# Performance work log

Hardware: AMD Instinct MI355X
Metric: run time of the kernel (lower is better)

## Reference

```python
import jax, jax.numpy as jnp
import numpy as np

N_NODES = 50000
N_EDGES = 800000
C = 96
L = 3


def setup_inputs() -> dict:
    key = jax.random.key(0)
    ks = jax.random.split(key, 7)
    x = jax.random.normal(ks[0], (N_NODES, C), dtype=jnp.float32)
    edge_index = jax.random.randint(ks[1], (2, N_EDGES), 0, N_NODES, dtype=jnp.int32)
    weight = jax.random.normal(ks[2], (L, C, C), dtype=jnp.float32) * (1.0 / np.sqrt(C))
    w_ih = jax.random.normal(ks[3], (3 * C, C), dtype=jnp.float32) * (1.0 / np.sqrt(C))
    w_hh = jax.random.normal(ks[4], (3 * C, C), dtype=jnp.float32) * (1.0 / np.sqrt(C))
    b_ih = jax.random.normal(ks[5], (3 * C,), dtype=jnp.float32) * 0.01
    b_hh = jax.random.normal(ks[6], (3 * C,), dtype=jnp.float32) * 0.01
    return {"x": x, "edge_index": edge_index, "weight": weight,
            "w_ih": w_ih, "w_hh": w_hh, "b_ih": b_ih, "b_hh": b_hh}


def _gru_cell(m, h, w_ih, w_hh, b_ih, b_hh):
    # PyTorch GRUCell math. gi/gh: [N, 3C]
    gi = m @ w_ih.T + b_ih
    gh = h @ w_hh.T + b_hh
    i_r, i_z, i_n = jnp.split(gi, 3, axis=-1)
    h_r, h_z, h_n = jnp.split(gh, 3, axis=-1)
    r = jax.nn.sigmoid(i_r + h_r)
    z = jax.nn.sigmoid(i_z + h_z)
    n = jnp.tanh(i_n + r * h_n)
    return (1.0 - z) * n + z * h


def reference(x, edge_index, weight, w_ih, w_hh, b_ih, b_hh):
    src = edge_index[0]  # message source (x_j)
    dst = edge_index[1]  # aggregation target
    for i in range(L):
        m = x @ weight[i]                                        # [N, C]
        agg = jax.ops.segment_sum(m[src], dst, num_segments=N_NODES)  # scatter-add
        x = _gru_cell(agg, x, w_ih, w_hh, b_ih, b_hh)
    return x
```

## Files before the change

### kernel.cpp

```cpp
#include <hip/hip_runtime.h>
#include <hip/hip_bf16.h>
#include <stdint.h>

#define NN 50000
#define NE 800000
#define CC 96
#define NL 3
#define NMT 3125

#define CAP 64
#define CAPSH 6

#define ELEMS_PER_LAYER 55296

#define FILL_GROUPS 8
#define FILL_GROUP_BLOCKS 400
#define FILL_BLOCKS (FILL_GROUPS*FILL_GROUP_BLOCKS)
#define NODES_PER_GROUP (NN/FILL_GROUPS)

#define PREP_ITEMS (NN*CC/8 + NL*288*CC + 288*CC)
#define PREP_BLOCKS ((PREP_ITEMS + 255)/256)

typedef _Float16 f16x8 __attribute__((ext_vector_type(8)));
typedef float f32x4 __attribute__((ext_vector_type(4)));
typedef uint16_t u16x8 __attribute__((ext_vector_type(8)));

__device__ __forceinline__ uint16_t f2h(float f){
  _Float16 h = (_Float16)f;
  return __builtin_bit_cast(uint16_t, h);
}
__device__ __forceinline__ float h2f(uint16_t u){
  return (float)__builtin_bit_cast(_Float16, u);
}

__device__ __forceinline__ size_t frag_elem(int tcol, int g2, int ks, int lane, int j){
  return (((size_t)(tcol*6 + g2)*3 + ks)*64 + lane)*8 + j;
}

__global__ void k_setup(const int* __restrict__ srcv, const int* __restrict__ dstv,
                        int* __restrict__ cursor, uint16_t* __restrict__ ssrc,
                        const float4* __restrict__ x, u16x8* __restrict__ xh,
                        const float* __restrict__ weight, const float* __restrict__ w_ih,
                        const float* __restrict__ w_hh, uint16_t* __restrict__ gw){
  if(blockIdx.x < FILL_BLOCKS){
    int g  = blockIdx.x & 7;
    int bg = blockIdx.x >> 3;
    int dlo = g * NODES_PER_GROUP;
    int dhi = dlo + NODES_PER_GROUP;
    const int tpg = FILL_GROUP_BLOCKS*256;
    for(int e = bg*256 + threadIdx.x; e < NE; e += tpg){
      int d = dstv[e];
      if(d >= dlo && d < dhi){
        int s = srcv[e];
        int pos = atomicAdd(&cursor[d], 1);
        if(pos < CAP) ssrc[((size_t)d << CAPSH) + pos] = (uint16_t)s;
      }
    }
    return;
  }
  int idx = (blockIdx.x - FILL_BLOCKS)*256 + threadIdx.x;
  const int N8 = NN*CC/8;
  if(idx < N8){
    float4 a = x[idx*2], b = x[idx*2+1];
    u16x8 o;
    o[0]=f2h(a.x); o[1]=f2h(a.y); o[2]=f2h(a.z); o[3]=f2h(a.w);
    o[4]=f2h(b.x); o[5]=f2h(b.y); o[6]=f2h(b.z); o[7]=f2h(b.w);
    xh[idx] = o;
    return;
  }
  int pidx = idx - N8;
  const int TOT1 = NL*288*CC;
  const int TOT2 = 288*CC;
  if(pidx < TOT1){
    int k = pidx % CC;
    int col = (pidx / CC) % 288;
    int l = pidx / (CC*288);
    const float4* wr = (const float4*)(weight + (size_t)(l*CC + k)*CC);
    const float4* ir = (const float4*)(w_ih + (size_t)col*CC);
    float acc = 0.f;
    #pragma unroll 4
    for(int k2=0;k2<CC/4;k2++){
      float4 a = wr[k2], b = ir[k2];
      acc += a.x*b.x + a.y*b.y + a.z*b.z + a.w*b.w;
    }
    int g = col / 96, cg = col % 96;
    int tcol = cg >> 4, n = cg & 15;
    int ks = k >> 5, r = (k & 31) >> 3, j = k & 7;
    int lane = r*16 + n;
    gw[(size_t)l*ELEMS_PER_LAYER + frag_elem(tcol, g, ks, lane, j)] = f2h(acc);
  } else {
    int idx2 = pidx - TOT1;
    if(idx2 < TOT2){
      int k = idx2 % CC;
      int col = idx2 / CC;
      uint16_t h = f2h(w_hh[(size_t)col*CC + k]);
      int g = col / 96, cg = col % 96;
      int tcol = cg >> 4, n = cg & 15;
      int ks = k >> 5, r = (k & 31) >> 3, j = k & 7;
      int lane = r*16 + n;
      size_t fe = frag_elem(tcol, 3+g, ks, lane, j);
      #pragma unroll
      for(int l=0;l<NL;l++) gw[(size_t)l*ELEMS_PER_LAYER + fe] = h;
    }
  }
}

__global__ void k_aggregate(const u16x8* __restrict__ xh,
                            const int* __restrict__ counts, const uint16_t* __restrict__ ssrc,
                            u16x8* __restrict__ s16){
  int tid = blockIdx.x*256 + threadIdx.x;
  if(tid >= NN*12) return;
  int n = tid / 12;
  int c8 = tid - n*12;
  int cnt = counts[n];
  if(cnt > CAP) cnt = CAP;
  int o0 = n << CAPSH;
  int o1 = o0 + cnt;
  float a[8];
  #pragma unroll
  for(int t=0;t<8;t++) a[t] = 0.f;
  int j = o0;
  for(; j+8 <= o1; j+=8){
    int s0 = ssrc[j],   s1 = ssrc[j+1], s2 = ssrc[j+2], s3 = ssrc[j+3];
    int s4 = ssrc[j+4], s5 = ssrc[j+5], s6 = ssrc[j+6], s7 = ssrc[j+7];
    u16x8 v0 = xh[(size_t)s0*12 + c8];
    u16x8 v1 = xh[(size_t)s1*12 + c8];
    u16x8 v2 = xh[(size_t)s2*12 + c8];
    u16x8 v3 = xh[(size_t)s3*12 + c8];
    u16x8 v4 = xh[(size_t)s4*12 + c8];
    u16x8 v5 = xh[(size_t)s5*12 + c8];
    u16x8 v6 = xh[(size_t)s6*12 + c8];
    u16x8 v7 = xh[(size_t)s7*12 + c8];
    #pragma unroll
    for(int t=0;t<8;t++)
      a[t] += ((h2f(v0[t])+h2f(v1[t]))+(h2f(v2[t])+h2f(v3[t])))
            + ((h2f(v4[t])+h2f(v5[t]))+(h2f(v6[t])+h2f(v7[t])));
  }
  for(; j < o1; j++){
    u16x8 v = xh[(size_t)ssrc[j]*12 + c8];
    #pragma unroll
    for(int t=0;t<8;t++) a[t] += h2f(v[t]);
  }
  u16x8 o;
  #pragma unroll
  for(int t=0;t<8;t++) o[t] = f2h(a[t]);
  s16[tid] = o;
}

#define MFMA16(A,B,C) __builtin_amdgcn_mfma_f32_16x16x32_f16(A,B,C,0,0,0)

__global__ __launch_bounds__(1024) void k_gru(
    const uint16_t* __restrict__ s16, uint16_t* xh,
    const uint16_t* __restrict__ gw_l,
    const float* __restrict__ b_ih, const float* __restrict__ b_hh,
    float* __restrict__ out_f)
{
  __shared__ __align__(16) uint16_t lw[ELEMS_PER_LAYER];

  const int tid = threadIdx.x;
  int wave = tid >> 6;
  int lane = tid & 63;
  int mtile = wave*256 + blockIdx.x;
  bool valid = (mtile < NMT);
  int mt = valid ? mtile : 0;
  int nidx = lane & 15;
  int quad = lane >> 4;

  f16x8 as[3], ax[3];
  {
    size_t arow = (size_t)(mt*16 + nidx)*CC;
    #pragma unroll
    for(int ks=0; ks<3; ks++){
      int ko = ks*32 + quad*8;
      as[ks] = *reinterpret_cast<const f16x8*>(s16 + arow + ko);
      ax[ks] = *reinterpret_cast<const f16x8*>(xh + arow + ko);
    }
  }

  {
    const uint4* src = (const uint4*)gw_l;
    uint4* dst = (uint4*)lw;
    #pragma unroll
    for(int i=0;i<7;i++){
      int chunk = i*1024 + tid;
      if(chunk < ELEMS_PER_LAYER/8) dst[chunk] = src[chunk];
    }
  }
  __syncthreads();
  if(!valid) return;

  #pragma unroll 1
  for(int tcol=0; tcol<6; tcol++){
    f32x4 air = {0.f,0.f,0.f,0.f}, aiz = {0.f,0.f,0.f,0.f}, ain = {0.f,0.f,0.f,0.f};
    f32x4 ahr = {0.f,0.f,0.f,0.f}, ahz = {0.f,0.f,0.f,0.f}, ahn = {0.f,0.f,0.f,0.f};

    #pragma unroll
    for(int ks=0; ks<3; ks++){
      const uint16_t* base = lw + (((size_t)tcol*6)*3 + ks)*512 + lane*8;
      #define BFRAG(g2) (*reinterpret_cast<const f16x8*>(base + (size_t)(g2)*3*512))
      air = MFMA16(as[ks], BFRAG(0), air);
      aiz = MFMA16(as[ks], BFRAG(1), aiz);
      ain = MFMA16(as[ks], BFRAG(2), ain);
      ahr = MFMA16(ax[ks], BFRAG(3), ahr);
      ahz = MFMA16(ax[ks], BFRAG(4), ahz);
      ahn = MFMA16(ax[ks], BFRAG(5), ahn);
      #undef BFRAG
    }

    int c = tcol*16 + nidx;
    float bir_ = b_ih[c], biz_ = b_ih[CC+c], bin_ = b_ih[2*CC+c];
    float bhr_ = b_hh[c], bhz_ = b_hh[CC+c], bhn_ = b_hh[2*CC+c];

    #pragma unroll
    for(int r=0;r<4;r++){
      int node = mtile*16 + quad*4 + r;
      float ir  = air[r] + bir_;
      float iz  = aiz[r] + biz_;
      float in_ = ain[r] + bin_;
      float hr  = ahr[r] + bhr_;
      float hz  = ahz[r] + bhz_;
      float hn  = ahn[r] + bhn_;
      float rg = 1.f/(1.f + __expf(-(ir+hr)));
      float zg = 1.f/(1.f + __expf(-(iz+hz)));
      float nv = in_ + rg*hn;
      float av = fminf(fabsf(nv), 15.f);
      float e2 = __expf(2.f*av);
      float tg = 1.f - 2.f/(e2 + 1.f);
      tg = (nv < 0.f)? -tg : tg;
      size_t oi = (size_t)node*CC + c;
      float hp = h2f(xh[oi]);
      float h = (1.f - zg)*tg + zg*hp;
      if(out_f) out_f[oi] = h;
      else      xh[oi] = f2h(h);
    }
  }
}

extern "C" void kernel_launch(void* const* d_in, const int* in_sizes, int n_in,
                              void* d_out, int out_size, void* d_ws, size_t ws_size,
                              hipStream_t stream){
  const float* x0     = (const float*)d_in[0];
  const int*   ei     = (const int*)d_in[1];
  const float* weight = (const float*)d_in[2];
  const float* w_ih   = (const float*)d_in[3];
  const float* w_hh   = (const float*)d_in[4];
  const float* b_ih   = (const float*)d_in[5];
  const float* b_hh   = (const float*)d_in[6];
  float* out = (float*)d_out;

  const int* srcv = ei;
  const int* dstv = ei + NE;

  char* ws = (char*)d_ws;
  size_t off = 0;
  auto carve = [&](size_t bytes)->char*{
    char* p = ws + off;
    off += (bytes + 255) & ~(size_t)255;
    return p;
  };
  int* cursor    = (int*)carve((size_t)NN*4);
  uint16_t* ssrc = (uint16_t*)carve((size_t)NN*CAP*2);
  uint16_t* s16  = (uint16_t*)carve((size_t)NN*CC*2);
  uint16_t* xh   = (uint16_t*)carve((size_t)NN*CC*2);
  uint16_t* gw   = (uint16_t*)carve((size_t)NL*ELEMS_PER_LAYER*2);

  hipMemsetAsync(cursor, 0, (size_t)NN*4, stream);
  k_setup<<<FILL_BLOCKS + PREP_BLOCKS, 256, 0, stream>>>(
      srcv, dstv, cursor, ssrc, (const float4*)x0, (u16x8*)xh, weight, w_ih, w_hh, gw);

  for(int l=0; l<NL; l++){
    k_aggregate<<<((NN*12)+255)/256, 256, 0, stream>>>(
        (const u16x8*)xh, cursor, ssrc, (u16x8*)s16);
    float* out_f = (l==NL-1) ? out : nullptr;
    k_gru<<<256, 1024, 0, stream>>>(s16, xh,
                                    gw + (size_t)l*ELEMS_PER_LAYER,
                                    b_ih, b_hh, out_f);
  }
}
```

Baseline: 275.7 us.

## Fuse neighbor aggregation into GRU layer kernel with ping-pong node buffers

Removes the separate aggregation kernel and performs the gather-sum inside the GRU kernel. Each thread sums three 8-channel chunks for one node, staging the results in shared memory as MFMA A-fragments. This avoids writing and re-reading the aggregated fp16 buffer in global memory and saves one launch per layer. Because other blocks still read the current node states while this layer writes new ones, the states now alternate between two buffers. The trade-off is fewer waves for the latency-bound gather and shared memory use close to the per-CU limit.

Result: faster. 256.6 us (-6.9%).

```diff
diff --git a/kernel.cpp b/kernel.cpp
--- a/kernel.cpp
+++ b/kernel.cpp
@@ -105,76 +105,33 @@
   }
 }
 
-__global__ void k_aggregate(const u16x8* __restrict__ xh,
-                            const int* __restrict__ counts, const uint16_t* __restrict__ ssrc,
-                            u16x8* __restrict__ s16){
-  int tid = blockIdx.x*256 + threadIdx.x;
-  if(tid >= NN*12) return;
-  int n = tid / 12;
-  int c8 = tid - n*12;
-  int cnt = counts[n];
-  if(cnt > CAP) cnt = CAP;
-  int o0 = n << CAPSH;
-  int o1 = o0 + cnt;
-  float a[8];
-  #pragma unroll
-  for(int t=0;t<8;t++) a[t] = 0.f;
-  int j = o0;
-  for(; j+8 <= o1; j+=8){
-    int s0 = ssrc[j],   s1 = ssrc[j+1], s2 = ssrc[j+2], s3 = ssrc[j+3];
-    int s4 = ssrc[j+4], s5 = ssrc[j+5], s6 = ssrc[j+6], s7 = ssrc[j+7];
-    u16x8 v0 = xh[(size_t)s0*12 + c8];
-    u16x8 v1 = xh[(size_t)s1*12 + c8];
-    u16x8 v2 = xh[(size_t)s2*12 + c8];
-    u16x8 v3 = xh[(size_t)s3*12 + c8];
-    u16x8 v4 = xh[(size_t)s4*12 + c8];
-    u16x8 v5 = xh[(size_t)s5*12 + c8];
-    u16x8 v6 = xh[(size_t)s6*12 + c8];
-    u16x8 v7 = xh[(size_t)s7*12 + c8];
-    #pragma unroll
-    for(int t=0;t<8;t++)
-      a[t] += ((h2f(v0[t])+h2f(v1[t]))+(h2f(v2[t])+h2f(v3[t])))
-            + ((h2f(v4[t])+h2f(v5[t]))+(h2f(v6[t])+h2f(v7[t])));
-  }
-  for(; j < o1; j++){
-    u16x8 v = xh[(size_t)ssrc[j]*12 + c8];
-    #pragma unroll
-    for(int t=0;t<8;t++) a[t] += h2f(v[t]);
-  }
-  u16x8 o;
-  #pragma unroll
-  for(int t=0;t<8;t++) o[t] = f2h(a[t]);
-  s16[tid] = o;
-}
-
 #define MFMA16(A,B,C) __builtin_amdgcn_mfma_f32_16x16x32_f16(A,B,C,0,0,0)
 
-__global__ __launch_bounds__(1024) void k_gru(
-    const uint16_t* __restrict__ s16, uint16_t* xh,
+__global__ __launch_bounds__(1024) void k_layer(
+    const uint16_t* __restrict__ xh_cur, uint16_t* __restrict__ xh_nxt,
+    const int* __restrict__ counts, const uint16_t* __restrict__ ssrc,
     const uint16_t* __restrict__ gw_l,
     const float* __restrict__ b_ih, const float* __restrict__ b_hh,
     float* __restrict__ out_f)
 {
   __shared__ __align__(16) uint16_t lw[ELEMS_PER_LAYER];
+  __shared__ u16x8 aggl[12*256];
 
   const int tid = threadIdx.x;
-  int wave = tid >> 6;
-  int lane = tid & 63;
-  int mtile = wave*256 + blockIdx.x;
-  bool valid = (mtile < NMT);
-  int mt = valid ? mtile : 0;
-  int nidx = lane & 15;
-  int quad = lane >> 4;
-
-  f16x8 as[3], ax[3];
+  const int wave = tid >> 6;
+  const int lane = tid & 63;
+  const int nidx = lane & 15;
+  const int quad = lane >> 4;
+  const int mtile = wave*256 + blockIdx.x;
+  const bool valid = (mtile < NMT);
+  const int mt = valid ? mtile : 0;
+
+  f16x8 ax[3];
   {
     size_t arow = (size_t)(mt*16 + nidx)*CC;
     #pragma unroll
-    for(int ks=0; ks<3; ks++){
-      int ko = ks*32 + quad*8;
-      as[ks] = *reinterpret_cast<const f16x8*>(s16 + arow + ko);
-      ax[ks] = *reinterpret_cast<const f16x8*>(xh + arow + ko);
-    }
+    for(int ks=0; ks<3; ks++)
+      ax[ks] = *reinterpret_cast<const f16x8*>(xh_cur + arow + ks*32 + quad*8);
   }
 
   {
@@ -186,8 +143,58 @@
       if(chunk < ELEMS_PER_LAYER/8) dst[chunk] = src[chunk];
     }
   }
+
+  {
+    int nl_ = tid >> 2;
+    int c8b = (tid & 3)*3;
+    if(valid){
+      int node = mt*16 + (nl_ & 15);
+      int cnt = counts[node]; if(cnt > CAP) cnt = CAP;
+      const u16x8* xg = (const u16x8*)xh_cur;
+      float a0[8], a1[8], a2[8];
+      #pragma unroll
+      for(int t=0;t<8;t++){ a0[t]=0.f; a1[t]=0.f; a2[t]=0.f; }
+      int j0 = node << CAPSH;
+      int j1 = j0 + cnt;
+      int j = j0;
+      for(; j+4 <= j1; j+=4){
+        ushort4 sv = *reinterpret_cast<const ushort4*>(ssrc + j);
+        size_t b0 = (size_t)sv.x*12 + c8b;
+        size_t b1 = (size_t)sv.y*12 + c8b;
+        size_t b2 = (size_t)sv.z*12 + c8b;
+        size_t b3 = (size_t)sv.w*12 + c8b;
+        u16x8 v00=xg[b0], v01=xg[b0+1], v02=xg[b0+2];
+        u16x8 v10=xg[b1], v11=xg[b1+1], v12=xg[b1+2];
+        u16x8 v20=xg[b2], v21=xg[b2+1], v22=xg[b2+2];
+        u16x8 v30=xg[b3], v31=xg[b3+1], v32=xg[b3+2];
+        #pragma unroll
+        for(int t=0;t<8;t++){
+          a0[t] += (h2f(v00[t])+h2f(v10[t])) + (h2f(v20[t])+h2f(v30[t]));
+          a1[t] += (h2f(v01[t])+h2f(v11[t])) + (h2f(v21[t])+h2f(v31[t]));
+          a2[t] += (h2f(v02[t])+h2f(v12[t])) + (h2f(v22[t])+h2f(v32[t]));
+        }
+      }
+      for(; j < j1; j++){
+        size_t b = (size_t)ssrc[j]*12 + c8b;
+        u16x8 v0=xg[b], v1=xg[b+1], v2=xg[b+2];
+        #pragma unroll
+        for(int t=0;t<8;t++){ a0[t]+=h2f(v0[t]); a1[t]+=h2f(v1[t]); a2[t]+=h2f(v2[t]); }
+      }
+      u16x8 w0, w1, w2;
+      #pragma unroll
+      for(int t=0;t<8;t++){ w0[t]=f2h(a0[t]); w1[t]=f2h(a1[t]); w2[t]=f2h(a2[t]); }
+      aggl[(c8b+0)*256 + nl_] = w0;
+      aggl[(c8b+1)*256 + nl_] = w1;
+      aggl[(c8b+2)*256 + nl_] = w2;
+    }
+  }
   __syncthreads();
   if(!valid) return;
+
+  f16x8 as[3];
+  #pragma unroll
+  for(int ks=0; ks<3; ks++)
+    as[ks] = *reinterpret_cast<const f16x8*>(&aggl[(ks*4+quad)*256 + wave*16 + nidx]);
 
   #pragma unroll 1
   for(int tcol=0; tcol<6; tcol++){
@@ -228,10 +235,10 @@
       float tg = 1.f - 2.f/(e2 + 1.f);
       tg = (nv < 0.f)? -tg : tg;
       size_t oi = (size_t)node*CC + c;
-      float hp = h2f(xh[oi]);
+      float hp = h2f(xh_cur[oi]);
       float h = (1.f - zg)*tg + zg*hp;
       if(out_f) out_f[oi] = h;
-      else      xh[oi] = f2h(h);
+      else      xh_nxt[oi] = f2h(h);
     }
   }
 }
@@ -258,22 +265,23 @@
     off += (bytes + 255) & ~(size_t)255;
     return p;
   };
-  int* cursor    = (int*)carve((size_t)NN*4);
-  uint16_t* ssrc = (uint16_t*)carve((size_t)NN*CAP*2);
-  uint16_t* s16  = (uint16_t*)carve((size_t)NN*CC*2);
-  uint16_t* xh   = (uint16_t*)carve((size_t)NN*CC*2);
-  uint16_t* gw   = (uint16_t*)carve((size_t)NL*ELEMS_PER_LAYER*2);
+  int* cursor     = (int*)carve((size_t)NN*4);
+  uint16_t* ssrc  = (uint16_t*)carve((size_t)NN*CAP*2);
+  uint16_t* xh16A = (uint16_t*)carve((size_t)NN*CC*2);
+  uint16_t* xh16B = (uint16_t*)carve((size_t)NN*CC*2);
+  uint16_t* gw    = (uint16_t*)carve((size_t)NL*ELEMS_PER_LAYER*2);
 
   hipMemsetAsync(cursor, 0, (size_t)NN*4, stream);
   k_setup<<<FILL_BLOCKS + PREP_BLOCKS, 256, 0, stream>>>(
-      srcv, dstv, cursor, ssrc, (const float4*)x0, (u16x8*)xh, weight, w_ih, w_hh, gw);
-
+      srcv, dstv, cursor, ssrc, (const float4*)x0, (u16x8*)xh16A, weight, w_ih, w_hh, gw);
+
+  uint16_t* xh_cur = xh16A;
+  uint16_t* xh_nxt = xh16B;
   for(int l=0; l<NL; l++){
-    k_aggregate<<<((NN*12)+255)/256, 256, 0, stream>>>(
-        (const u16x8*)xh, cursor, ssrc, (u16x8*)s16);
     float* out_f = (l==NL-1) ? out : nullptr;
-    k_gru<<<256, 1024, 0, stream>>>(s16, xh,
-                                    gw + (size_t)l*ELEMS_PER_LAYER,
-                                    b_ih, b_hh, out_f);
-  }
-}
+    k_layer<<<256, 1024, 0, stream>>>(xh_cur, xh_nxt, cursor, ssrc,
+                                      gw + (size_t)l*ELEMS_PER_LAYER,
+                                      b_ih, b_hh, out_f);
+    uint16_t* t = xh_cur; xh_cur = xh_nxt; xh_nxt = t;
+  }
+}
```
